# Kernel optimization log

Hardware: AMD Instinct MI355X
Metric: run time of the kernel (lower is better)

## Reference

```python
import jax, jax.numpy as jnp
import numpy as np

HEADS = 2
D_IN = 100
K = 50
SCALE = 100.0 ** 0.25  # applied to both q and k -> effective 1/sqrt(100)


def setup_inputs() -> dict:
    key = jax.random.key(0)
    ks = jax.random.split(key, 7)
    b, t = 8, 2048
    x = jax.random.normal(ks[0], (b, t, D_IN), dtype=jnp.float32)
    mask = jax.random.normal(ks[1], (b, t), dtype=jnp.float32)
    s = 1.0 / np.sqrt(D_IN)
    Wq = jax.random.normal(ks[2], (D_IN, HEADS * K), dtype=jnp.float32) * s
    Wk = jax.random.normal(ks[3], (D_IN, HEADS * K), dtype=jnp.float32) * s
    Wv = jax.random.normal(ks[4], (D_IN, HEADS * K), dtype=jnp.float32) * s
    Wo = jax.random.normal(ks[5], (HEADS * K, D_IN), dtype=jnp.float32) * (1.0 / np.sqrt(HEADS * K))
    bo = jnp.zeros((D_IN,), dtype=jnp.float32)
    return {"x": x, "mask": mask, "Wq": Wq, "Wk": Wk, "Wv": Wv, "Wo": Wo, "bo": bo}


def reference(x, mask, Wq, Wk, Wv, Wo, bo):
    b, t, _ = x.shape
    H, k = HEADS, K
    # project and split heads: (b, t, H, k) -> (b, H, t, k)
    q = (x @ Wq).reshape(b, t, H, k).transpose(0, 2, 1, 3) / SCALE
    kk = (x @ Wk).reshape(b, t, H, k).transpose(0, 2, 1, 3) / SCALE
    v = (x @ Wv).reshape(b, t, H, k).transpose(0, 2, 1, 3)
    scores = jnp.einsum('bhtk,bhsk->bhts', q, kk)  # (b, H, t, t)
    # replicate torch.cat([mask, mask], dim=0) mapped onto (b, H) row-major flat index
    m = jnp.concatenate([mask, mask], axis=0).reshape(b, H, t)
    scores = scores + m[:, :, None, :]
    w = jax.nn.softmax(scores, axis=-1)
    ctx = jnp.einsum('bhts,bhsk->bhtk', w, v)  # (b, H, t, k)
    ctx = ctx.transpose(0, 2, 1, 3).reshape(b, t, H * k)
    return x + ctx @ Wo + bo
```

## Files before the change

kernel.cpp:

```cpp
#include <hip/hip_runtime.h>
#include <hip/hip_bf16.h>
#include <math.h>


#define BATCH 8
#define SEQ   2048
#define DIN   100
#define NH    2
#define KR    50
#define KD    64
#define BH    16
#define SPLIT 2
#define KSPAN (SEQ / SPLIT)

typedef __attribute__((ext_vector_type(8))) short short8;
typedef __attribute__((ext_vector_type(4))) short short4v;
typedef __attribute__((ext_vector_type(4))) float float4v;
typedef __attribute__((ext_vector_type(2))) float float2v;

__device__ inline short f2bf(float f) {
    __hip_bfloat16 h = __float2bfloat16(f);
    return *reinterpret_cast<short*>(&h);
}
__device__ inline float bf2f(short s) {
    __hip_bfloat16 h;
    *reinterpret_cast<short*>(&h) = s;
    return __bfloat162float(h);
}
__device__ inline float faddf(float a, float b) { return a + b; }

#define DPP_STEP(v, ctrl, OP) \
    v = OP(v, __int_as_float(__builtin_amdgcn_mov_dpp(__float_as_int(v), ctrl, 0xF, 0xF, true)))
#define RED16(v, OP) do { \
    DPP_STEP(v, 0xB1, OP); DPP_STEP(v, 0x4E, OP); \
    DPP_STEP(v, 0x124, OP); DPP_STEP(v, 0x128, OP); } while (0)

#define OFF_QF   0u
#define OFF_KF   4194304u
#define OFF_VF   8388608u
#define OFF_OP   12582912u
#define OFF_ML   20971520u
#define OFF_WTF  21495808u
#define OFF_WOTF 21594112u

#define N_WT  49152
#define N_WOT 14336
#define N_PREP (N_WT + N_WOT)

__global__ __launch_bounds__(256) void prep(
        const float* __restrict__ Wq, const float* __restrict__ Wk,
        const float* __restrict__ Wv, const float* __restrict__ Wo,
        short* __restrict__ wtf, short* __restrict__ wotf) {
    for (int i = blockIdx.x * 256 + threadIdx.x; i < N_PREP; i += gridDim.x * 256) {
        if (i < N_WT) {
            int n = i >> 7, k = i & 127;
            float val = 0.0f;
            if (k < DIN) {
                if (n < 256) {
                    int proj = n >> 7, h = (n >> 6) & 1, kk = n & 63;
                    if (kk < KR)
                        val = (proj ? Wk : Wq)[k * DIN + h * KR + kk] * (proj ? 1.0f : 0.1f);
                } else {
                    int vv = n - 256, h = vv >> 6, kk = vv & 63;
                    if (kk < KR) val = Wv[k * DIN + h * KR + kk];
                }
            }
            int nb = n >> 4, n16 = n & 15, c = k >> 5, q2 = (k >> 3) & 3, j = k & 7;
            wtf[(((nb * 4 + c) * 64) + q2 * 16 + n16) * 8 + j] = f2bf(val);
        } else {
            int e = i - N_WT, n = e >> 7, k = e & 127;
            float val = (n < DIN && k < DIN) ? Wo[k * DIN + n] : 0.0f;
            int nb = n >> 4, n16 = n & 15, c = k >> 5, q2 = (k >> 3) & 3, j = k & 7;
            wotf[(((nb * 4 + c) * 64) + q2 * 16 + n16) * 8 + j] = f2bf(val);
        }
    }
}

__global__ __launch_bounds__(256, 4) void qkv_gemm(
        const float* __restrict__ x, const short* __restrict__ wtf,
        const float* __restrict__ mask,
        short* __restrict__ qf, short* __restrict__ kf, short* __restrict__ vf) {
    __shared__ __align__(16) short xs[64 * 136];
    __shared__ __align__(16) short ls[64 * 72];
    const int m0 = blockIdx.x * 64, by = blockIdx.y, n0 = by * 64;
    const int tid = threadIdx.x;
    const int wave = tid >> 6, lane = tid & 63, quad = lane >> 4, n16 = lane & 15;

    {
        const int r = tid >> 2, seg = tid & 3;
        const float* xr = x + (size_t)(m0 + r) * DIN;
        if (seg < 3) {
#pragma unroll
            for (int q8 = 0; q8 < 4; q8++) {
                float4v a = *(const float4v*)(xr + seg * 32 + q8 * 8);
                float4v b = *(const float4v*)(xr + seg * 32 + q8 * 8 + 4);
                short8 s8;
#pragma unroll
                for (int j = 0; j < 4; j++) { s8[j] = f2bf(a[j]); s8[4 + j] = f2bf(b[j]); }
                *(short8*)&xs[r * 136 + seg * 32 + q8 * 8] = s8;
            }
        } else {
            float4v a = *(const float4v*)(xr + 96);
            short8 s8 = {0, 0, 0, 0, 0, 0, 0, 0};
#pragma unroll
            for (int j = 0; j < 4; j++) s8[j] = f2bf(a[j]);
            *(short8*)&xs[r * 136 + 96] = s8;
            short8 z = {0, 0, 0, 0, 0, 0, 0, 0};
            *(short8*)&xs[r * 136 + 104] = z;
            *(short8*)&xs[r * 136 + 112] = z;
            *(short8*)&xs[r * 136 + 120] = z;
        }
    }
    __syncthreads();

    float4v acc[4];
#pragma unroll
    for (int nt = 0; nt < 4; nt++) { acc[nt][0] = 0.f; acc[nt][1] = 0.f; acc[nt][2] = 0.f; acc[nt][3] = 0.f; }

#pragma unroll
    for (int ks = 0; ks < 4; ks++) {
        short8 af = *(const short8*)&xs[(wave * 16 + n16) * 136 + ks * 32 + quad * 8];
#pragma unroll
        for (int nt = 0; nt < 4; nt++) {
            short8 bf = *(const short8*)&wtf[((((n0 >> 4) + nt) * 4 + ks) * 64 + lane) * 8];
            acc[nt] = __builtin_amdgcn_mfma_f32_16x16x32_bf16(af, bf, acc[nt], 0, 0, 0);
        }
    }

    const int bi = m0 >> 11, tb0 = m0 & 2047;
    const int h = by & 1, bh = bi * NH + h;

    if (by < 4) {
        const bool isq = (by < 2);
        const float* mrow = mask + (size_t)(bh & 7) * SEQ + tb0;
#pragma unroll
        for (int nt = 0; nt < 4; nt++) {
#pragma unroll
            for (int r = 0; r < 4; r++) {
                float val = acc[nt][r];
                if (nt == 3 && n16 == 2)
                    val = isq ? 1.0f : mrow[wave * 16 + quad * 4 + r];
                ls[(wave * 16 + quad * 4 + r) * 72 + nt * 16 + n16] = f2bf(val);
            }
        }
        __syncthreads();
        short* dst = (isq ? qf : kf) + ((size_t)(bh * 128 + (tb0 >> 4) + wave) * 2) * 512;
#pragma unroll
        for (int c = 0; c < 2; c++) {
            short8 fr = *(const short8*)&ls[(wave * 16 + n16) * 72 + c * 32 + quad * 8];
            *(short8*)&dst[c * 512 + lane * 8] = fr;
        }
    } else {
#pragma unroll
        for (int nt = 0; nt < 4; nt++) {
            short4v s4;
#pragma unroll
            for (int r = 0; r < 4; r++) s4[r] = f2bf(acc[nt][r]);
            *(short4v*)&ls[(nt * 16 + n16) * 72 + wave * 16 + quad * 4] = s4;
        }
        __syncthreads();
        short* dst = vf + ((size_t)(bh * 4 + wave) * 64 + (tb0 >> 5)) * 512;
#pragma unroll
        for (int kc = 0; kc < 2; kc++) {
            short8 fr = *(const short8*)&ls[(wave * 16 + n16) * 72 + kc * 32 + quad * 8];
            *(short8*)&dst[kc * 512 + lane * 8] = fr;
        }
    }
}

__global__ __launch_bounds__(256, 3) void attn(
        const short* __restrict__ qf, const short* __restrict__ kf,
        const short* __restrict__ vf,
        short* __restrict__ o_part, float2v* __restrict__ ml) {
    __shared__ __align__(16) short P[4][16 * 72];

    const int bh = blockIdx.x;
    const int t0 = blockIdx.y * 64;
    const int sp = blockIdx.z;
    const int tid = threadIdx.x;
    const int wave = tid >> 6, lane = tid & 63, quad = lane >> 4, n16 = lane & 15;

    const short* qfb = qf + ((size_t)(bh * 128 + (t0 >> 4) + wave) * 2) * 512;
    const short8 qa0 = *(const short8*)&qfb[lane * 8];
    const short8 qa1 = *(const short8*)&qfb[512 + lane * 8];

    const short* kfb = kf + (size_t)bh * 128 * 2 * 512;
    const short* vfb = vf + (size_t)bh * 4 * 64 * 512;
    short* Pw = &P[wave][0];

    float mold[4], lold[4];
#pragma unroll
    for (int r = 0; r < 4; r++) { mold[r] = -INFINITY; lold[r] = 0.0f; }
    float4v oc[4];
#pragma unroll
    for (int nt = 0; nt < 4; nt++) { oc[nt][0] = 0.f; oc[nt][1] = 0.f; oc[nt][2] = 0.f; oc[nt][3] = 0.f; }

    for (int s0 = sp * KSPAN; s0 < sp * KSPAN + KSPAN; s0 += 64) {
        const int sb = s0 >> 4, kcb = s0 >> 5;
        short8 kfr[4][2], vfr[4][2];
#pragma unroll
        for (int jb = 0; jb < 4; jb++) {
#pragma unroll
            for (int c = 0; c < 2; c++)
                kfr[jb][c] = *(const short8*)&kfb[((sb + jb) * 2 + c) * 512 + lane * 8];
        }
#pragma unroll
        for (int nt = 0; nt < 4; nt++) {
#pragma unroll
            for (int kc = 0; kc < 2; kc++)
                vfr[nt][kc] = *(const short8*)&vfb[(nt * 64 + kcb + kc) * 512 + lane * 8];
        }

        float4v cf[4];
#pragma unroll
        for (int jb = 0; jb < 4; jb++) {
            float4v z = {0.f, 0.f, 0.f, 0.f};
            z = __builtin_amdgcn_mfma_f32_16x16x32_bf16(qa0, kfr[jb][0], z, 0, 0, 0);
            z = __builtin_amdgcn_mfma_f32_16x16x32_bf16(qa1, kfr[jb][1], z, 0, 0, 0);
            cf[jb] = z;
        }

        float mnew[4], al[4], rsum[4];
#pragma unroll
        for (int r = 0; r < 4; r++) {
            float rmax = fmaxf(fmaxf(cf[0][r], cf[1][r]), fmaxf(cf[2][r], cf[3][r]));
            RED16(rmax, fmaxf);
            mnew[r] = fmaxf(mold[r], rmax);
            al[r]   = __expf(mold[r] - mnew[r]);
            mold[r] = mnew[r];
            rsum[r] = 0.0f;
        }
#pragma unroll
        for (int jb = 0; jb < 4; jb++) {
#pragma unroll
            for (int r = 0; r < 4; r++) {
                float p = __expf(cf[jb][r] - mnew[r]);
                rsum[r] += p;
                Pw[(quad * 4 + r) * 72 + jb * 16 + n16] = f2bf(p);
            }
        }
#pragma unroll
        for (int r = 0; r < 4; r++) {
            RED16(rsum[r], faddf);
            lold[r] = lold[r] * al[r] + rsum[r];
        }

#pragma unroll
        for (int nt = 0; nt < 4; nt++) {
#pragma unroll
            for (int r = 0; r < 4; r++) oc[nt][r] *= al[r];
        }
        short8 pa0 = *(const short8*)&Pw[n16 * 72 + quad * 8];
        short8 pa1 = *(const short8*)&Pw[n16 * 72 + 32 + quad * 8];
#pragma unroll
        for (int nt = 0; nt < 4; nt++) {
            oc[nt] = __builtin_amdgcn_mfma_f32_16x16x32_bf16(pa0, vfr[nt][0], oc[nt], 0, 0, 0);
            oc[nt] = __builtin_amdgcn_mfma_f32_16x16x32_bf16(pa1, vfr[nt][1], oc[nt], 0, 0, 0);
        }
    }

    float linv[4];
#pragma unroll
    for (int r = 0; r < 4; r++) linv[r] = 1.0f / lold[r];
    short* ob = o_part + (size_t)((sp * BH + bh) * KD) * SEQ;
#pragma unroll
    for (int nt = 0; nt < 4; nt++) {
        short4v s4;
#pragma unroll
        for (int r = 0; r < 4; r++) s4[r] = f2bf(oc[nt][r] * linv[r]);
        *(short4v*)&ob[(size_t)(nt * 16 + n16) * SEQ + t0 + wave * 16 + quad * 4] = s4;
    }
    if (n16 == 0) {
#pragma unroll
        for (int r = 0; r < 4; r++) {
            float2v v2; v2[0] = mold[r]; v2[1] = lold[r];
            ml[(size_t)(sp * BH + bh) * SEQ + t0 + wave * 16 + quad * 4 + r] = v2;
        }
    }
}

__global__ __launch_bounds__(256, 4) void out_proj(
        const float* __restrict__ x, const short* __restrict__ o_part,
        const float2v* __restrict__ ml, const short* __restrict__ wotf,
        const float* __restrict__ bo, float* __restrict__ out) {
    __shared__ __align__(16) short as[64 * 136];
    __shared__ float css[SPLIT][128];

    const int g0 = blockIdx.x * 64;
    const int bi = g0 >> 11, tb = g0 & 2047;
    const int tid = threadIdx.x;
    const int wave = tid >> 6, lane = tid & 63, quad = lane >> 4, n16 = lane & 15;

    if (tid < 128) {
        int r = tid >> 1, h = tid & 1;
        int bh = bi * NH + h, t = tb + r;
        float mm[SPLIT], ll[SPLIT], m = -INFINITY;
#pragma unroll
        for (int s = 0; s < SPLIT; s++) {
            float2v a = ml[(size_t)(s * BH + bh) * SEQ + t];
            mm[s] = a[0]; ll[s] = a[1];
            m = fmaxf(m, mm[s]);
        }
        float w[SPLIT], wsum = 0.0f;
#pragma unroll
        for (int s = 0; s < SPLIT; s++) { w[s] = ll[s] * __expf(mm[s] - m); wsum += w[s]; }
        float inv = 1.0f / wsum;
#pragma unroll
        for (int s = 0; s < SPLIT; s++) css[s][tid] = w[s] * inv;
    }
    __syncthreads();

    for (int e = tid; e < 64 * 128; e += 256) {
        int r = e >> 7, i = e & 127;
        float val = 0.0f;
        if (i < DIN) {
            int h = (i >= KR) ? 1 : 0, kd = i - h * KR;
            int bh = bi * NH + h, t = tb + r;
#pragma unroll
            for (int s = 0; s < SPLIT; s++)
                val += css[s][r * 2 + h] *
                       bf2f(o_part[(size_t)((s * BH + bh) * KD + kd) * SEQ + t]);
        }
        as[r * 136 + i] = f2bf(val);
    }
    __syncthreads();

    float4v acc[7];
#pragma unroll
    for (int nt = 0; nt < 7; nt++) { acc[nt][0] = 0.f; acc[nt][1] = 0.f; acc[nt][2] = 0.f; acc[nt][3] = 0.f; }

#pragma unroll
    for (int ks = 0; ks < 4; ks++) {
        short8 af = *(const short8*)&as[(wave * 16 + n16) * 136 + ks * 32 + quad * 8];
#pragma unroll
        for (int nt = 0; nt < 7; nt++) {
            short8 bf = *(const short8*)&wotf[((nt * 4 + ks) * 64 + lane) * 8];
            acc[nt] = __builtin_amdgcn_mfma_f32_16x16x32_bf16(af, bf, acc[nt], 0, 0, 0);
        }
    }

#pragma unroll
    for (int nt = 0; nt < 7; nt++) {
        int col = nt * 16 + n16;
        if (col < DIN) {
            float bv = bo[col];
#pragma unroll
            for (int r = 0; r < 4; r++) {
                int row = wave * 16 + quad * 4 + r;
                size_t idx = (size_t)(g0 + row) * DIN + col;
                out[idx] = x[idx] + acc[nt][r] + bv;
            }
        }
    }
}

extern "C" void kernel_launch(void* const* d_in, const int* in_sizes, int n_in,
                              void* d_out, int out_size, void* d_ws, size_t ws_size,
                              hipStream_t stream) {
    const float* x    = (const float*)d_in[0];
    const float* mask = (const float*)d_in[1];
    const float* Wq   = (const float*)d_in[2];
    const float* Wk   = (const float*)d_in[3];
    const float* Wv   = (const float*)d_in[4];
    const float* Wo   = (const float*)d_in[5];
    const float* bo   = (const float*)d_in[6];
    float* out = (float*)d_out;

    char* ws = (char*)d_ws;
    short*   qfp    = (short*)(ws + OFF_QF);
    short*   kfp    = (short*)(ws + OFF_KF);
    short*   vfp    = (short*)(ws + OFF_VF);
    short*   o_part = (short*)(ws + OFF_OP);
    float2v* mlv    = (float2v*)(ws + OFF_ML);
    short*   wtf    = (short*)(ws + OFF_WTF);
    short*   wotf   = (short*)(ws + OFF_WOTF);

    prep<<<128, 256, 0, stream>>>(Wq, Wk, Wv, Wo, wtf, wotf);
    qkv_gemm<<<dim3(256, 6), 256, 0, stream>>>(x, wtf, mask, qfp, kfp, vfp);
    attn<<<dim3(BH, SEQ / 64, SPLIT), 256, 0, stream>>>(qfp, kfp, vfp, o_part, mlv);
    out_proj<<<256, 256, 0, stream>>>(x, o_part, mlv, wotf, bo, out);
}
```

Measured before the change: 140.1 us.

## Rework attention pipeline: exp2 softmax, row-sum via ones column, larger tiles, fragment layouts

Folds log2(e) into the Q weights so softmax can use exp2. The row sum is computed by the PV MFMA through a column of ones appended to V, which removes the DPP sum reduction. Each attention wave now processes two 16-row query tiles per K/V load to reuse the loaded fragments, and the key split can be 4 when the workspace is large enough. qkv_gemm computes three projection groups per block, reusing the x fragments. out_proj reads the split outputs in MFMA fragment layout directly into registers, with no LDS staging. Bit-twiddling bf16 conversion replaces the library calls; this rounding ignores NaN handling, and the larger per-wave register state may reduce occupancy.

```diff
diff --git a/kernel.cpp b/kernel.cpp
--- a/kernel.cpp
+++ b/kernel.cpp
@@ -10,38 +10,35 @@
 #define KR    50
 #define KD    64
 #define BH    16
-#define SPLIT 2
-#define KSPAN (SEQ / SPLIT)
+#define LOG2E 1.44269504f
 
 typedef __attribute__((ext_vector_type(8))) short short8;
-typedef __attribute__((ext_vector_type(4))) short short4v;
 typedef __attribute__((ext_vector_type(4))) float float4v;
 typedef __attribute__((ext_vector_type(2))) float float2v;
+typedef __attribute__((ext_vector_type(2))) unsigned uint2v;
 
 __device__ inline short f2bf(float f) {
     __hip_bfloat16 h = __float2bfloat16(f);
     return *reinterpret_cast<short*>(&h);
 }
 __device__ inline float bf2f(short s) {
-    __hip_bfloat16 h;
-    *reinterpret_cast<short*>(&h) = s;
-    return __bfloat162float(h);
-}
-__device__ inline float faddf(float a, float b) { return a + b; }
+    unsigned u = ((unsigned)(unsigned short)s) << 16;
+    return __uint_as_float(u);
+}
+__device__ inline short b16r(float f) {
+    return (short)((__float_as_uint(f) + 0x8000u) >> 16);
+}
+__device__ inline unsigned pk2(float lo, float hi) {
+    unsigned ul = __float_as_uint(lo) + 0x8000u;
+    unsigned uh = __float_as_uint(hi) + 0x8000u;
+    return __builtin_amdgcn_perm(uh, ul, 0x07060302u);
+}
 
 #define DPP_STEP(v, ctrl, OP) \
     v = OP(v, __int_as_float(__builtin_amdgcn_mov_dpp(__float_as_int(v), ctrl, 0xF, 0xF, true)))
 #define RED16(v, OP) do { \
     DPP_STEP(v, 0xB1, OP); DPP_STEP(v, 0x4E, OP); \
     DPP_STEP(v, 0x124, OP); DPP_STEP(v, 0x128, OP); } while (0)
-
-#define OFF_QF   0u
-#define OFF_KF   4194304u
-#define OFF_VF   8388608u
-#define OFF_OP   12582912u
-#define OFF_ML   20971520u
-#define OFF_WTF  21495808u
-#define OFF_WOTF 21594112u
 
 #define N_WT  49152
 #define N_WOT 14336
@@ -59,7 +56,8 @@
                 if (n < 256) {
                     int proj = n >> 7, h = (n >> 6) & 1, kk = n & 63;
                     if (kk < KR)
-                        val = (proj ? Wk : Wq)[k * DIN + h * KR + kk] * (proj ? 1.0f : 0.1f);
+                        val = (proj ? Wk : Wq)[k * DIN + h * KR + kk] *
+                              (proj ? 1.0f : 0.1f * LOG2E);
                 } else {
                     int vv = n - 256, h = vv >> 6, kk = vv & 63;
                     if (kk < KR) val = Wv[k * DIN + h * KR + kk];
@@ -69,20 +67,21 @@
             wtf[(((nb * 4 + c) * 64) + q2 * 16 + n16) * 8 + j] = f2bf(val);
         } else {
             int e = i - N_WT, n = e >> 7, k = e & 127;
-            float val = (n < DIN && k < DIN) ? Wo[k * DIN + n] : 0.0f;
+            int h = k >> 6, kd = k & 63;
+            float val = (n < DIN && kd < KR) ? Wo[(h * KR + kd) * DIN + n] : 0.0f;
             int nb = n >> 4, n16 = n & 15, c = k >> 5, q2 = (k >> 3) & 3, j = k & 7;
             wotf[(((nb * 4 + c) * 64) + q2 * 16 + n16) * 8 + j] = f2bf(val);
         }
     }
 }
 
-__global__ __launch_bounds__(256, 4) void qkv_gemm(
+__global__ __launch_bounds__(256) void qkv_gemm(
         const float* __restrict__ x, const short* __restrict__ wtf,
         const float* __restrict__ mask,
         short* __restrict__ qf, short* __restrict__ kf, short* __restrict__ vf) {
     __shared__ __align__(16) short xs[64 * 136];
     __shared__ __align__(16) short ls[64 * 72];
-    const int m0 = blockIdx.x * 64, by = blockIdx.y, n0 = by * 64;
+    const int m0 = blockIdx.x * 64;
     const int tid = threadIdx.x;
     const int wave = tid >> 6, lane = tid & 63, quad = lane >> 4, n16 = lane & 15;
 
@@ -94,17 +93,17 @@
             for (int q8 = 0; q8 < 4; q8++) {
                 float4v a = *(const float4v*)(xr + seg * 32 + q8 * 8);
                 float4v b = *(const float4v*)(xr + seg * 32 + q8 * 8 + 4);
-                short8 s8;
-#pragma unroll
-                for (int j = 0; j < 4; j++) { s8[j] = f2bf(a[j]); s8[4 + j] = f2bf(b[j]); }
-                *(short8*)&xs[r * 136 + seg * 32 + q8 * 8] = s8;
+                union { unsigned u[4]; short8 s; } t;
+                t.u[0] = pk2(a[0], a[1]); t.u[1] = pk2(a[2], a[3]);
+                t.u[2] = pk2(b[0], b[1]); t.u[3] = pk2(b[2], b[3]);
+                *(short8*)&xs[r * 136 + seg * 32 + q8 * 8] = t.s;
             }
         } else {
             float4v a = *(const float4v*)(xr + 96);
-            short8 s8 = {0, 0, 0, 0, 0, 0, 0, 0};
-#pragma unroll
-            for (int j = 0; j < 4; j++) s8[j] = f2bf(a[j]);
-            *(short8*)&xs[r * 136 + 96] = s8;
+            union { unsigned u[4]; short8 s; } t;
+            t.u[0] = pk2(a[0], a[1]); t.u[1] = pk2(a[2], a[3]);
+            t.u[2] = 0; t.u[3] = 0;
+            *(short8*)&xs[r * 136 + 96] = t.s;
             short8 z = {0, 0, 0, 0, 0, 0, 0, 0};
             *(short8*)&xs[r * 136 + 104] = z;
             *(short8*)&xs[r * 136 + 112] = z;
@@ -113,87 +112,102 @@
     }
     __syncthreads();
 
-    float4v acc[4];
-#pragma unroll
-    for (int nt = 0; nt < 4; nt++) { acc[nt][0] = 0.f; acc[nt][1] = 0.f; acc[nt][2] = 0.f; acc[nt][3] = 0.f; }
-
-#pragma unroll
-    for (int ks = 0; ks < 4; ks++) {
-        short8 af = *(const short8*)&xs[(wave * 16 + n16) * 136 + ks * 32 + quad * 8];
-#pragma unroll
-        for (int nt = 0; nt < 4; nt++) {
-            short8 bf = *(const short8*)&wtf[((((n0 >> 4) + nt) * 4 + ks) * 64 + lane) * 8];
-            acc[nt] = __builtin_amdgcn_mfma_f32_16x16x32_bf16(af, bf, acc[nt], 0, 0, 0);
-        }
-    }
+    short8 xa[4];
+#pragma unroll
+    for (int ks = 0; ks < 4; ks++)
+        xa[ks] = *(const short8*)&xs[(wave * 16 + n16) * 136 + ks * 32 + quad * 8];
 
     const int bi = m0 >> 11, tb0 = m0 & 2047;
-    const int h = by & 1, bh = bi * NH + h;
-
-    if (by < 4) {
-        const bool isq = (by < 2);
-        const float* mrow = mask + (size_t)(bh & 7) * SEQ + tb0;
-#pragma unroll
-        for (int nt = 0; nt < 4; nt++) {
-#pragma unroll
-            for (int r = 0; r < 4; r++) {
-                float val = acc[nt][r];
-                if (nt == 3 && n16 == 2)
-                    val = isq ? 1.0f : mrow[wave * 16 + quad * 4 + r];
-                ls[(wave * 16 + quad * 4 + r) * 72 + nt * 16 + n16] = f2bf(val);
-            }
-        }
+
+    for (int bys = 0; bys < 3; bys++) {
+        const int by = blockIdx.y * 3 + bys;
+        float4v acc[4];
+#pragma unroll
+        for (int nt = 0; nt < 4; nt++) { acc[nt][0] = 0.f; acc[nt][1] = 0.f; acc[nt][2] = 0.f; acc[nt][3] = 0.f; }
+#pragma unroll
+        for (int ks = 0; ks < 4; ks++) {
+#pragma unroll
+            for (int nt = 0; nt < 4; nt++) {
+                short8 bf = *(const short8*)&wtf[(((by * 4 + nt) * 4 + ks) * 64 + lane) * 8];
+                acc[nt] = __builtin_amdgcn_mfma_f32_16x16x32_bf16(xa[ks], bf, acc[nt], 0, 0, 0);
+            }
+        }
+        const int h = by & 1, bh = bi * NH + h;
         __syncthreads();
-        short* dst = (isq ? qf : kf) + ((size_t)(bh * 128 + (tb0 >> 4) + wave) * 2) * 512;
-#pragma unroll
-        for (int c = 0; c < 2; c++) {
-            short8 fr = *(const short8*)&ls[(wave * 16 + n16) * 72 + c * 32 + quad * 8];
-            *(short8*)&dst[c * 512 + lane * 8] = fr;
-        }
-    } else {
-#pragma unroll
-        for (int nt = 0; nt < 4; nt++) {
-            short4v s4;
-#pragma unroll
-            for (int r = 0; r < 4; r++) s4[r] = f2bf(acc[nt][r]);
-            *(short4v*)&ls[(nt * 16 + n16) * 72 + wave * 16 + quad * 4] = s4;
+
+        if (by < 4) {
+            const bool isq = (by < 2);
+            const float* mrow = mask + (size_t)(bh & 7) * SEQ + tb0;
+#pragma unroll
+            for (int nt = 0; nt < 4; nt++) {
+#pragma unroll
+                for (int r = 0; r < 4; r++) {
+                    float val = acc[nt][r];
+                    if (nt == 3 && n16 == 2)
+                        val = isq ? LOG2E : mrow[wave * 16 + quad * 4 + r];
+                    ls[(wave * 16 + quad * 4 + r) * 72 + nt * 16 + n16] = b16r(val);
+                }
+            }
+            __syncthreads();
+            short* dst = (isq ? qf : kf) + ((size_t)(bh * 128 + (tb0 >> 4) + wave) * 2) * 512;
+#pragma unroll
+            for (int c = 0; c < 2; c++)
+                *(short8*)&dst[c * 512 + lane * 8] =
+                    *(const short8*)&ls[(wave * 16 + n16) * 72 + c * 32 + quad * 8];
+        } else {
+#pragma unroll
+            for (int nt = 0; nt < 4; nt++) {
+                float v0 = acc[nt][0], v1 = acc[nt][1], v2 = acc[nt][2], v3 = acc[nt][3];
+                if (nt == 3 && n16 == 2) { v0 = 1.f; v1 = 1.f; v2 = 1.f; v3 = 1.f; }
+                uint2v u; u[0] = pk2(v0, v1); u[1] = pk2(v2, v3);
+                *(uint2v*)&ls[(nt * 16 + n16) * 72 + wave * 16 + quad * 4] = u;
+            }
+            __syncthreads();
+            short* dst = vf + ((size_t)(bh * 4 + wave) * 64 + (tb0 >> 5)) * 512;
+#pragma unroll
+            for (int kc = 0; kc < 2; kc++)
+                *(short8*)&dst[kc * 512 + lane * 8] =
+                    *(const short8*)&ls[(wave * 16 + n16) * 72 + kc * 32 + quad * 8];
         }
         __syncthreads();
-        short* dst = vf + ((size_t)(bh * 4 + wave) * 64 + (tb0 >> 5)) * 512;
-#pragma unroll
-        for (int kc = 0; kc < 2; kc++) {
-            short8 fr = *(const short8*)&ls[(wave * 16 + n16) * 72 + kc * 32 + quad * 8];
-            *(short8*)&dst[kc * 512 + lane * 8] = fr;
-        }
-    }
-}
-
-__global__ __launch_bounds__(256, 3) void attn(
+    }
+}
+
+template <int S>
+__global__ __launch_bounds__(256) void attn(
         const short* __restrict__ qf, const short* __restrict__ kf,
         const short* __restrict__ vf,
         short* __restrict__ o_part, float2v* __restrict__ ml) {
-    __shared__ __align__(16) short P[4][16 * 72];
+    __shared__ __align__(16) short P[4][2][16 * 72];
 
     const int bh = blockIdx.x;
-    const int t0 = blockIdx.y * 64;
+    const int t0 = blockIdx.y * 128;
     const int sp = blockIdx.z;
+    const int KSPAN = SEQ / S;
     const int tid = threadIdx.x;
     const int wave = tid >> 6, lane = tid & 63, quad = lane >> 4, n16 = lane & 15;
 
-    const short* qfb = qf + ((size_t)(bh * 128 + (t0 >> 4) + wave) * 2) * 512;
-    const short8 qa0 = *(const short8*)&qfb[lane * 8];
-    const short8 qa1 = *(const short8*)&qfb[512 + lane * 8];
+    short8 qa[2][2];
+#pragma unroll
+    for (int s = 0; s < 2; s++) {
+        const short* qfb = qf + ((size_t)(bh * 128 + (t0 >> 4) + wave * 2 + s) * 2) * 512;
+        qa[s][0] = *(const short8*)&qfb[lane * 8];
+        qa[s][1] = *(const short8*)&qfb[512 + lane * 8];
+    }
+
+    float mold[2][4];
+    float4v oc[2][4];
+#pragma unroll
+    for (int s = 0; s < 2; s++)
+#pragma unroll
+        for (int r = 0; r < 4; r++) mold[s][r] = -INFINITY;
+#pragma unroll
+    for (int s = 0; s < 2; s++)
+#pragma unroll
+        for (int nt = 0; nt < 4; nt++) { oc[s][nt][0] = 0.f; oc[s][nt][1] = 0.f; oc[s][nt][2] = 0.f; oc[s][nt][3] = 0.f; }
 
     const short* kfb = kf + (size_t)bh * 128 * 2 * 512;
     const short* vfb = vf + (size_t)bh * 4 * 64 * 512;
-    short* Pw = &P[wave][0];
-
-    float mold[4], lold[4];
-#pragma unroll
-    for (int r = 0; r < 4; r++) { mold[r] = -INFINITY; lold[r] = 0.0f; }
-    float4v oc[4];
-#pragma unroll
-    for (int nt = 0; nt < 4; nt++) { oc[nt][0] = 0.f; oc[nt][1] = 0.f; oc[nt][2] = 0.f; oc[nt][3] = 0.f; }
 
     for (int s0 = sp * KSPAN; s0 < sp * KSPAN + KSPAN; s0 += 64) {
         const int sb = s0 >> 4, kcb = s0 >> 5;
@@ -211,143 +225,155 @@
                 vfr[nt][kc] = *(const short8*)&vfb[(nt * 64 + kcb + kc) * 512 + lane * 8];
         }
 
-        float4v cf[4];
-#pragma unroll
-        for (int jb = 0; jb < 4; jb++) {
-            float4v z = {0.f, 0.f, 0.f, 0.f};
-            z = __builtin_amdgcn_mfma_f32_16x16x32_bf16(qa0, kfr[jb][0], z, 0, 0, 0);
-            z = __builtin_amdgcn_mfma_f32_16x16x32_bf16(qa1, kfr[jb][1], z, 0, 0, 0);
-            cf[jb] = z;
-        }
-
-        float mnew[4], al[4], rsum[4];
+#pragma unroll
+        for (int s = 0; s < 2; s++) {
+            float4v cf[4];
+#pragma unroll
+            for (int jb = 0; jb < 4; jb++) {
+                float4v z = {0.f, 0.f, 0.f, 0.f};
+                z = __builtin_amdgcn_mfma_f32_16x16x32_bf16(qa[s][0], kfr[jb][0], z, 0, 0, 0);
+                z = __builtin_amdgcn_mfma_f32_16x16x32_bf16(qa[s][1], kfr[jb][1], z, 0, 0, 0);
+                cf[jb] = z;
+            }
+            float mnew[4], al[4];
+#pragma unroll
+            for (int r = 0; r < 4; r++) {
+                float rmax = fmaxf(fmaxf(cf[0][r], cf[1][r]), fmaxf(cf[2][r], cf[3][r]));
+                RED16(rmax, fmaxf);
+                mnew[r] = fmaxf(mold[s][r], rmax);
+                al[r]   = __builtin_amdgcn_exp2f(mold[s][r] - mnew[r]);
+                mold[s][r] = mnew[r];
+            }
+            short* Pw = &P[wave][s][0];
+#pragma unroll
+            for (int jb = 0; jb < 4; jb++) {
+#pragma unroll
+                for (int r = 0; r < 4; r++) {
+                    float p = __builtin_amdgcn_exp2f(cf[jb][r] - mnew[r]);
+                    Pw[(quad * 4 + r) * 72 + jb * 16 + n16] = b16r(p);
+                }
+            }
+#pragma unroll
+            for (int nt = 0; nt < 4; nt++) {
+#pragma unroll
+                for (int r = 0; r < 4; r++) oc[s][nt][r] *= al[r];
+            }
+            short8 pa0 = *(const short8*)&Pw[n16 * 72 + quad * 8];
+            short8 pa1 = *(const short8*)&Pw[n16 * 72 + 32 + quad * 8];
+#pragma unroll
+            for (int nt = 0; nt < 4; nt++) {
+                oc[s][nt] = __builtin_amdgcn_mfma_f32_16x16x32_bf16(pa0, vfr[nt][0], oc[s][nt], 0, 0, 0);
+                oc[s][nt] = __builtin_amdgcn_mfma_f32_16x16x32_bf16(pa1, vfr[nt][1], oc[s][nt], 0, 0, 0);
+            }
+        }
+    }
+
+#pragma unroll
+    for (int s = 0; s < 2; s++) {
+        float lv[4], linv[4];
 #pragma unroll
         for (int r = 0; r < 4; r++) {
-            float rmax = fmaxf(fmaxf(cf[0][r], cf[1][r]), fmaxf(cf[2][r], cf[3][r]));
-            RED16(rmax, fmaxf);
-            mnew[r] = fmaxf(mold[r], rmax);
-            al[r]   = __expf(mold[r] - mnew[r]);
-            mold[r] = mnew[r];
-            rsum[r] = 0.0f;
-        }
-#pragma unroll
-        for (int jb = 0; jb < 4; jb++) {
+            lv[r] = __shfl(oc[s][3][r], quad * 16 + 2, 64);
+            linv[r] = 1.0f / lv[r];
+        }
+        short* Pw = &P[wave][s][0];
+#pragma unroll
+        for (int nt = 0; nt < 4; nt++) {
+#pragma unroll
+            for (int r = 0; r < 4; r++)
+                Pw[(quad * 4 + r) * 72 + nt * 16 + n16] = b16r(oc[s][nt][r] * linv[r]);
+        }
+        short* ob = o_part + ((size_t)((sp * BH + bh) * 128 + (t0 >> 4) + wave * 2 + s) * 2) * 512;
+#pragma unroll
+        for (int c = 0; c < 2; c++)
+            *(short8*)&ob[c * 512 + lane * 8] =
+                *(const short8*)&Pw[n16 * 72 + c * 32 + quad * 8];
+        if (n16 == 0) {
 #pragma unroll
             for (int r = 0; r < 4; r++) {
-                float p = __expf(cf[jb][r] - mnew[r]);
-                rsum[r] += p;
-                Pw[(quad * 4 + r) * 72 + jb * 16 + n16] = f2bf(p);
-            }
-        }
-#pragma unroll
-        for (int r = 0; r < 4; r++) {
-            RED16(rsum[r], faddf);
-            lold[r] = lold[r] * al[r] + rsum[r];
-        }
-
-#pragma unroll
-        for (int nt = 0; nt < 4; nt++) {
-#pragma unroll
-            for (int r = 0; r < 4; r++) oc[nt][r] *= al[r];
-        }
-        short8 pa0 = *(const short8*)&Pw[n16 * 72 + quad * 8];
-        short8 pa1 = *(const short8*)&Pw[n16 * 72 + 32 + quad * 8];
-#pragma unroll
-        for (int nt = 0; nt < 4; nt++) {
-            oc[nt] = __builtin_amdgcn_mfma_f32_16x16x32_bf16(pa0, vfr[nt][0], oc[nt], 0, 0, 0);
-            oc[nt] = __builtin_amdgcn_mfma_f32_16x16x32_bf16(pa1, vfr[nt][1], oc[nt], 0, 0, 0);
-        }
-    }
-
-    float linv[4];
-#pragma unroll
-    for (int r = 0; r < 4; r++) linv[r] = 1.0f / lold[r];
-    short* ob = o_part + (size_t)((sp * BH + bh) * KD) * SEQ;
-#pragma unroll
-    for (int nt = 0; nt < 4; nt++) {
-        short4v s4;
-#pragma unroll
-        for (int r = 0; r < 4; r++) s4[r] = f2bf(oc[nt][r] * linv[r]);
-        *(short4v*)&ob[(size_t)(nt * 16 + n16) * SEQ + t0 + wave * 16 + quad * 4] = s4;
-    }
-    if (n16 == 0) {
-#pragma unroll
-        for (int r = 0; r < 4; r++) {
-            float2v v2; v2[0] = mold[r]; v2[1] = lold[r];
-            ml[(size_t)(sp * BH + bh) * SEQ + t0 + wave * 16 + quad * 4 + r] = v2;
-        }
-    }
-}
-
-__global__ __launch_bounds__(256, 4) void out_proj(
+                float2v v2; v2[0] = mold[s][r]; v2[1] = lv[r];
+                ml[(size_t)(sp * BH + bh) * SEQ + t0 + wave * 32 + s * 16 + quad * 4 + r] = v2;
+            }
+        }
+    }
+}
+
+template <int S>
+__global__ __launch_bounds__(128) void out_proj(
         const float* __restrict__ x, const short* __restrict__ o_part,
         const float2v* __restrict__ ml, const short* __restrict__ wotf,
         const float* __restrict__ bo, float* __restrict__ out) {
-    __shared__ __align__(16) short as[64 * 136];
-    __shared__ float css[SPLIT][128];
-
-    const int g0 = blockIdx.x * 64;
+    const int g0 = blockIdx.x * 32;
     const int bi = g0 >> 11, tb = g0 & 2047;
     const int tid = threadIdx.x;
     const int wave = tid >> 6, lane = tid & 63, quad = lane >> 4, n16 = lane & 15;
-
-    if (tid < 128) {
-        int r = tid >> 1, h = tid & 1;
-        int bh = bi * NH + h, t = tb + r;
-        float mm[SPLIT], ll[SPLIT], m = -INFINITY;
-#pragma unroll
-        for (int s = 0; s < SPLIT; s++) {
-            float2v a = ml[(size_t)(s * BH + bh) * SEQ + t];
+    const int trow = tb + wave * 16 + n16;
+
+    float cs[2][S];
+#pragma unroll
+    for (int h = 0; h < 2; h++) {
+        const int bh = bi * NH + h;
+        float mm[S], ll[S], mx = -INFINITY;
+#pragma unroll
+        for (int s = 0; s < S; s++) {
+            float2v a = ml[(size_t)(s * BH + bh) * SEQ + trow];
             mm[s] = a[0]; ll[s] = a[1];
-            m = fmaxf(m, mm[s]);
-        }
-        float w[SPLIT], wsum = 0.0f;
-#pragma unroll
-        for (int s = 0; s < SPLIT; s++) { w[s] = ll[s] * __expf(mm[s] - m); wsum += w[s]; }
+            mx = fmaxf(mx, mm[s]);
+        }
+        float w[S], wsum = 0.0f;
+#pragma unroll
+        for (int s = 0; s < S; s++) {
+            w[s] = ll[s] * __builtin_amdgcn_exp2f(mm[s] - mx);
+            wsum += w[s];
+        }
         float inv = 1.0f / wsum;
 #pragma unroll
-        for (int s = 0; s < SPLIT; s++) css[s][tid] = w[s] * inv;
-    }
-    __syncthreads();
-
-    for (int e = tid; e < 64 * 128; e += 256) {
-        int r = e >> 7, i = e & 127;
-        float val = 0.0f;
-        if (i < DIN) {
-            int h = (i >= KR) ? 1 : 0, kd = i - h * KR;
-            int bh = bi * NH + h, t = tb + r;
-#pragma unroll
-            for (int s = 0; s < SPLIT; s++)
-                val += css[s][r * 2 + h] *
-                       bf2f(o_part[(size_t)((s * BH + bh) * KD + kd) * SEQ + t]);
-        }
-        as[r * 136 + i] = f2bf(val);
-    }
-    __syncthreads();
+        for (int s = 0; s < S; s++) cs[h][s] = w[s] * inv;
+    }
+
+    const int rb = (tb >> 4) + wave;
+    short8 af[4];
+#pragma unroll
+    for (int c = 0; c < 4; c++) {
+        const int h = c >> 1, cc = c & 1, bh = bi * NH + h;
+        float v[8];
+#pragma unroll
+        for (int j = 0; j < 8; j++) v[j] = 0.0f;
+#pragma unroll
+        for (int s = 0; s < S; s++) {
+            const short* opb = o_part + ((size_t)((s * BH + bh) * 128 + rb) * 2 + cc) * 512;
+            short8 f = *(const short8*)&opb[lane * 8];
+            float w = cs[h][s];
+#pragma unroll
+            for (int j = 0; j < 8; j++) v[j] += w * bf2f(f[j]);
+        }
+        union { unsigned u[4]; short8 s8; } t;
+#pragma unroll
+        for (int p = 0; p < 4; p++) t.u[p] = pk2(v[2 * p], v[2 * p + 1]);
+        af[c] = t.s8;
+    }
 
     float4v acc[7];
 #pragma unroll
     for (int nt = 0; nt < 7; nt++) { acc[nt][0] = 0.f; acc[nt][1] = 0.f; acc[nt][2] = 0.f; acc[nt][3] = 0.f; }
-
 #pragma unroll
     for (int ks = 0; ks < 4; ks++) {
-        short8 af = *(const short8*)&as[(wave * 16 + n16) * 136 + ks * 32 + quad * 8];
 #pragma unroll
         for (int nt = 0; nt < 7; nt++) {
             short8 bf = *(const short8*)&wotf[((nt * 4 + ks) * 64 + lane) * 8];
-            acc[nt] = __builtin_amdgcn_mfma_f32_16x16x32_bf16(af, bf, acc[nt], 0, 0, 0);
+            acc[nt] = __builtin_amdgcn_mfma_f32_16x16x32_bf16(af[ks], bf, acc[nt], 0, 0, 0);
         }
     }
 
 #pragma unroll
     for (int nt = 0; nt < 7; nt++) {
-        int col = nt * 16 + n16;
+        const int col = nt * 16 + n16;
         if (col < DIN) {
             float bv = bo[col];
 #pragma unroll
             for (int r = 0; r < 4; r++) {
-                int row = wave * 16 + quad * 4 + r;
-                size_t idx = (size_t)(g0 + row) * DIN + col;
+                int row = g0 + wave * 16 + quad * 4 + r;
+                size_t idx = (size_t)row * DIN + col;
                 out[idx] = x[idx] + acc[nt][r] + bv;
             }
         }
@@ -366,17 +392,29 @@
     const float* bo   = (const float*)d_in[6];
     float* out = (float*)d_out;
 
+    const size_t SZ_QKV = 3u * 4194304u;
+    const size_t SZ_OP1 = 4194304u;
+    const size_t SZ_ML1 = (size_t)BH * SEQ * 8u;
+    const size_t SZ_W   = (size_t)N_WT * 2 + (size_t)N_WOT * 2;
+    const size_t need4  = SZ_QKV + 4 * SZ_OP1 + 4 * SZ_ML1 + SZ_W;
+    const int S = (ws_size >= need4 + 65536) ? 4 : 2;
+
     char* ws = (char*)d_ws;
-    short*   qfp    = (short*)(ws + OFF_QF);
-    short*   kfp    = (short*)(ws + OFF_KF);
-    short*   vfp    = (short*)(ws + OFF_VF);
-    short*   o_part = (short*)(ws + OFF_OP);
-    float2v* mlv    = (float2v*)(ws + OFF_ML);
-    short*   wtf    = (short*)(ws + OFF_WTF);
-    short*   wotf   = (short*)(ws + OFF_WOTF);
+    short*   qfp    = (short*)(ws);
+    short*   kfp    = (short*)(ws + 4194304u);
+    short*   vfp    = (short*)(ws + 8388608u);
+    short*   o_part = (short*)(ws + SZ_QKV);
+    float2v* mlv    = (float2v*)(ws + SZ_QKV + (size_t)S * SZ_OP1);
+    short*   wtf    = (short*)(ws + SZ_QKV + (size_t)S * (SZ_OP1 + SZ_ML1));
+    short*   wotf   = wtf + N_WT;
 
     prep<<<128, 256, 0, stream>>>(Wq, Wk, Wv, Wo, wtf, wotf);
-    qkv_gemm<<<dim3(256, 6), 256, 0, stream>>>(x, wtf, mask, qfp, kfp, vfp);
-    attn<<<dim3(BH, SEQ / 64, SPLIT), 256, 0, stream>>>(qfp, kfp, vfp, o_part, mlv);
-    out_proj<<<256, 256, 0, stream>>>(x, o_part, mlv, wotf, bo, out);
-}
+    qkv_gemm<<<dim3(256, 2), 256, 0, stream>>>(x, wtf, mask, qfp, kfp, vfp);
+    if (S == 4) {
+        attn<4><<<dim3(BH, SEQ / 128, 4), 256, 0, stream>>>(qfp, kfp, vfp, o_part, mlv);
+        out_proj<4><<<512, 128, 0, stream>>>(x, o_part, mlv, wotf, bo, out);
+    } else {
+        attn<2><<<dim3(BH, SEQ / 128, 2), 256, 0, stream>>>(qfp, kfp, vfp, o_part, mlv);
+        out_proj<2><<<512, 128, 0, stream>>>(x, o_part, mlv, wotf, bo, out);
+    }
+}
```

Measured after the change: 130.3 us. -7.0%, faster.
